# Kernel optimization log

Hardware: AMD Instinct MI355X
Metric: run time of the kernel (lower is better)

Reference implementation:

```python
import jax, jax.numpy as jnp
import numpy as np

D_MODEL = 256
B, BS_ANT, UE_ANT, N_SC = 4, 64, 4, 512
LN_EPS = 1e-5


def _xavier(key, shape, gain):
    fan_out, fan_in = shape
    bound = gain * np.sqrt(6.0 / (fan_in + fan_out))
    return jax.random.uniform(key, shape, jnp.float32, -bound, bound)


def setup_inputs() -> dict:
    key = jax.random.key(0)
    ks = jax.random.split(key, 8)
    csi_real = jax.random.normal(ks[0], (B, BS_ANT, UE_ANT, N_SC), jnp.float32)
    csi_imag = jax.random.normal(ks[1], (B, BS_ANT, UE_ANT, N_SC), jnp.float32)
    return {
        "csi_real": csi_real,
        "csi_imag": csi_imag,
        "w_c": _xavier(ks[2], (D_MODEL, 2), 2.0),
        "b_c": jnp.zeros((D_MODEL,), jnp.float32),
        "w_s": _xavier(ks[3], (D_MODEL, 1), 1.0),
        "b_s": jnp.zeros((D_MODEL,), jnp.float32),
        "w_u": _xavier(ks[4], (D_MODEL, 1), 1.0),
        "b_u": jnp.zeros((D_MODEL,), jnp.float32),
        "w_f": _xavier(ks[5], (D_MODEL, 1), 1.0),
        "b_f": jnp.zeros((D_MODEL,), jnp.float32),
        "ln_gamma": jnp.ones((D_MODEL,), jnp.float32),
        "ln_beta": jnp.zeros((D_MODEL,), jnp.float32),
    }


def reference(csi_real, csi_imag, w_c, b_c, w_s, b_s, w_u, b_u, w_f, b_f, ln_gamma, ln_beta):
    bs_ant, ue_ant, n_sc = csi_real.shape[1], csi_real.shape[2], csi_real.shape[3]
    # complex projection: stack(real, imag) @ W_c^T + b_c, done without the stack
    x = csi_real[..., None] * w_c[:, 0] + csi_imag[..., None] * w_c[:, 1] + b_c  # [B,BS,UE,SC,D]
    # index embeddings computed on the small per-axis arange, then broadcast (same math
    # as projecting the fully-expanded index tensors, since the projection is affine)
    sp = jnp.arange(bs_ant, dtype=csi_real.dtype)[:, None] * w_s[:, 0] + b_s   # [BS,D]
    ue = jnp.arange(ue_ant, dtype=csi_real.dtype)[:, None] * w_u[:, 0] + b_u   # [UE,D]
    fr = jnp.arange(n_sc, dtype=csi_real.dtype)[:, None] * w_f[:, 0] + b_f     # [SC,D]
    x = x + sp[None, :, None, None, :] + ue[None, None, :, None, :] + fr[None, None, None, :, :]
    # LayerNorm over d_model
    mu = jnp.mean(x, axis=-1, keepdims=True)
    xc = x - mu
    var = jnp.mean(xc * xc, axis=-1, keepdims=True)
    x = xc * jax.lax.rsqrt(var + LN_EPS) * ln_gamma + ln_beta
    # dropout is identity in eval/reference mode
    return x
```

## Files before the change

kernel.cpp:

```cpp
#include <hip/hip_runtime.h>

#define D_MODEL 256
#define LN_EPS 1e-5f
#define NWAVES 8192
#define NITER  64

typedef float f4 __attribute__((ext_vector_type(4)));

__device__ __forceinline__ float rfl(float x) {
    return __uint_as_float(__builtin_amdgcn_readfirstlane(__float_as_uint(x)));
}

__global__ __launch_bounds__(256, 8) void csi_encoder_kernel(
    const float* __restrict__ csi_real,
    const float* __restrict__ csi_imag,
    const float* __restrict__ w_c,
    const float* __restrict__ b_c,
    const float* __restrict__ w_s,
    const float* __restrict__ b_s,
    const float* __restrict__ w_u,
    const float* __restrict__ b_u,
    const float* __restrict__ w_f,
    const float* __restrict__ b_f,
    const float* __restrict__ ln_gamma,
    const float* __restrict__ ln_beta,
    float* __restrict__ out)
{
    const int lane = threadIdx.x & 63;
    const int waveId = blockIdx.x * 4 + (threadIdx.x >> 6);
    const int w0 = __builtin_amdgcn_readfirstlane(waveId);

    const float fS = (float)(w0 & 511);
    const float fU = (float)((w0 >> 9) & 3);
    const int   b0 = (w0 >> 11) & 63;

    const int d0 = lane * 4;
    float a0[4], a1[4], aB[4], w2[4], gv[4], bv[4];
#pragma unroll
    for (int j = 0; j < 4; ++j) {
        const int d = d0 + j;
        a0[j] = w_c[d * 2 + 0];
        a1[j] = w_c[d * 2 + 1];
        aB[j] = w_s[d];
        const float bsum = b_c[d] + b_s[d] + b_u[d] + b_f[d];
        w2[j] = fmaf(fS, w_f[d], fmaf(fU, w_u[d], bsum));
        gv[j] = ln_gamma[d];
        bv[j] = ln_beta[d];
    }

    float p[14];
#pragma unroll
    for (int i = 0; i < 14; ++i) p[i] = 0.0f;
#pragma unroll
    for (int j = 0; j < 4; ++j) {
        p[0]  = fmaf(a0[j], a0[j], p[0]);
        p[1]  = fmaf(a1[j], a1[j], p[1]);
        p[2]  = fmaf(aB[j], aB[j], p[2]);
        p[3]  = fmaf(w2[j], w2[j], p[3]);
        p[4]  = fmaf(a0[j], a1[j], p[4]);
        p[5]  = fmaf(a0[j], aB[j], p[5]);
        p[6]  = fmaf(a0[j], w2[j], p[6]);
        p[7]  = fmaf(a1[j], aB[j], p[7]);
        p[8]  = fmaf(a1[j], w2[j], p[8]);
        p[9]  = fmaf(aB[j], w2[j], p[9]);
        p[10] += a0[j];
        p[11] += a1[j];
        p[12] += aB[j];
        p[13] += w2[j];
    }
#pragma unroll
    for (int off = 32; off >= 1; off >>= 1) {
#pragma unroll
        for (int i = 0; i < 14; ++i) p[i] += __shfl_xor(p[i], off, 64);
    }

    const float inv = 1.0f / 256.0f;
    const float E00 = rfl(p[0] * inv);
    const float E11 = rfl(p[1] * inv);
    const float EBB = rfl(p[2] * inv);
    const float E33 = rfl(p[3] * inv);
    const float F01 = rfl(2.0f * p[4] * inv);
    const float F0B = rfl(2.0f * p[5] * inv);
    const float F03 = rfl(2.0f * p[6] * inv);
    const float F1B = rfl(2.0f * p[7] * inv);
    const float F13 = rfl(2.0f * p[8] * inv);
    const float FB3 = rfl(2.0f * p[9] * inv);
    const float M0  = rfl(p[10] * inv);
    const float M1  = rfl(p[11] * inv);
    const float MB  = rfl(p[12] * inv);
    const float M3  = rfl(p[13] * inv);

    const float* __restrict__ cr = csi_real + w0;
    const float* __restrict__ ci = csi_imag + w0;
    float* __restrict__ op = out + (size_t)w0 * D_MODEL + d0;

#pragma unroll 4
    for (int i = 0; i < NITER; ++i) {
        const float re = cr[(size_t)i << 13];
        const float im = ci[(size_t)i << 13];
        const float fB = (float)((b0 + 4 * i) & 63);

        const float mu = fmaf(M0, re, fmaf(M1, im, fmaf(MB, fB, M3)));
        const float ms = fmaf(re, fmaf(E00, re, fmaf(F01, im, fmaf(F0B, fB, F03))),
                         fmaf(im, fmaf(E11, im, fmaf(F1B, fB, F13)),
                         fmaf(fB, fmaf(EBB, fB, FB3), E33)));
        const float var  = fmaf(-mu, mu, ms);
        const float rstd = rsqrtf(var + LN_EPS);

        f4 o;
#pragma unroll
        for (int k = 0; k < 4; ++k) {
            const float t = fmaf(re, a0[k], fmaf(im, a1[k], fmaf(fB, aB[k], w2[k])));
            o[k] = fmaf((t - mu) * rstd, gv[k], bv[k]);
        }
        __builtin_nontemporal_store(o, (f4*)(op + ((size_t)i << 13) * D_MODEL));
    }
}

extern "C" void kernel_launch(void* const* d_in, const int* in_sizes, int n_in,
                              void* d_out, int out_size, void* d_ws, size_t ws_size,
                              hipStream_t stream) {
    const float* csi_real = (const float*)d_in[0];
    const float* csi_imag = (const float*)d_in[1];
    const float* w_c      = (const float*)d_in[2];
    const float* b_c      = (const float*)d_in[3];
    const float* w_s      = (const float*)d_in[4];
    const float* b_s      = (const float*)d_in[5];
    const float* w_u      = (const float*)d_in[6];
    const float* b_u      = (const float*)d_in[7];
    const float* w_f      = (const float*)d_in[8];
    const float* b_f      = (const float*)d_in[9];
    const float* ln_gamma = (const float*)d_in[10];
    const float* ln_beta  = (const float*)d_in[11];
    float* out = (float*)d_out;

    csi_encoder_kernel<<<2048, 256, 0, stream>>>(
        csi_real, csi_imag, w_c, b_c, w_s, b_s, w_u, b_u, w_f, b_f,
        ln_gamma, ln_beta, out);
}
```

Baseline: 120.8 us.

## Assign fewer waves more rows each, folding UE index into per-row stats

Measured after the change: 158.3 us. 31.1% more time.

```diff
diff --git a/kernel.cpp b/kernel.cpp
--- a/kernel.cpp
+++ b/kernel.cpp
@@ -2,8 +2,8 @@
 
 #define D_MODEL 256
 #define LN_EPS 1e-5f
-#define NWAVES 8192
-#define NITER  64
+#define NWAVES 1024
+#define NITER  512
 
 typedef float f4 __attribute__((ext_vector_type(4)));
 
@@ -11,7 +11,7 @@
     return __uint_as_float(__builtin_amdgcn_readfirstlane(__float_as_uint(x)));
 }
 
-__global__ __launch_bounds__(256, 8) void csi_encoder_kernel(
+__global__ __launch_bounds__(256) void csi_encoder_kernel(
     const float* __restrict__ csi_real,
     const float* __restrict__ csi_imag,
     const float* __restrict__ w_c,
@@ -27,94 +27,134 @@
     float* __restrict__ out)
 {
     const int lane = threadIdx.x & 63;
-    const int waveId = blockIdx.x * 4 + (threadIdx.x >> 6);
-    const int w0 = __builtin_amdgcn_readfirstlane(waveId);
+    const int w0 = __builtin_amdgcn_readfirstlane(blockIdx.x * 4 + (threadIdx.x >> 6));
 
-    const float fS = (float)(w0 & 511);
-    const float fU = (float)((w0 >> 9) & 3);
-    const int   b0 = (w0 >> 11) & 63;
+    const float fS  = (float)(w0 & 511);
+    const int  bit9 = (w0 >> 9) & 1;
+    const float fU0 = (float)bit9;
+    const float fU1 = (float)(bit9 + 2);
 
     const int d0 = lane * 4;
-    float a0[4], a1[4], aB[4], w2[4], gv[4], bv[4];
+    float a0[4], a1[4], aU[4], aB[4], w2[4], gv[4], bv[4];
 #pragma unroll
     for (int j = 0; j < 4; ++j) {
         const int d = d0 + j;
         a0[j] = w_c[d * 2 + 0];
         a1[j] = w_c[d * 2 + 1];
+        aU[j] = w_u[d];
         aB[j] = w_s[d];
         const float bsum = b_c[d] + b_s[d] + b_u[d] + b_f[d];
-        w2[j] = fmaf(fS, w_f[d], fmaf(fU, w_u[d], bsum));
+        w2[j] = fmaf(fS, w_f[d], bsum);
         gv[j] = ln_gamma[d];
         bv[j] = ln_beta[d];
     }
 
-    float p[14];
+    float p[20];
 #pragma unroll
-    for (int i = 0; i < 14; ++i) p[i] = 0.0f;
+    for (int i = 0; i < 20; ++i) p[i] = 0.0f;
 #pragma unroll
     for (int j = 0; j < 4; ++j) {
         p[0]  = fmaf(a0[j], a0[j], p[0]);
         p[1]  = fmaf(a1[j], a1[j], p[1]);
-        p[2]  = fmaf(aB[j], aB[j], p[2]);
-        p[3]  = fmaf(w2[j], w2[j], p[3]);
-        p[4]  = fmaf(a0[j], a1[j], p[4]);
-        p[5]  = fmaf(a0[j], aB[j], p[5]);
-        p[6]  = fmaf(a0[j], w2[j], p[6]);
-        p[7]  = fmaf(a1[j], aB[j], p[7]);
-        p[8]  = fmaf(a1[j], w2[j], p[8]);
-        p[9]  = fmaf(aB[j], w2[j], p[9]);
-        p[10] += a0[j];
-        p[11] += a1[j];
-        p[12] += aB[j];
-        p[13] += w2[j];
+        p[2]  = fmaf(aU[j], aU[j], p[2]);
+        p[3]  = fmaf(aB[j], aB[j], p[3]);
+        p[4]  = fmaf(w2[j], w2[j], p[4]);
+        p[5]  = fmaf(a0[j], a1[j], p[5]);
+        p[6]  = fmaf(a0[j], aU[j], p[6]);
+        p[7]  = fmaf(a0[j], aB[j], p[7]);
+        p[8]  = fmaf(a0[j], w2[j], p[8]);
+        p[9]  = fmaf(a1[j], aU[j], p[9]);
+        p[10] = fmaf(a1[j], aB[j], p[10]);
+        p[11] = fmaf(a1[j], w2[j], p[11]);
+        p[12] = fmaf(aU[j], aB[j], p[12]);
+        p[13] = fmaf(aU[j], w2[j], p[13]);
+        p[14] = fmaf(aB[j], w2[j], p[14]);
+        p[15] += a0[j];
+        p[16] += a1[j];
+        p[17] += aU[j];
+        p[18] += aB[j];
+        p[19] += w2[j];
     }
 #pragma unroll
     for (int off = 32; off >= 1; off >>= 1) {
 #pragma unroll
-        for (int i = 0; i < 14; ++i) p[i] += __shfl_xor(p[i], off, 64);
+        for (int i = 0; i < 20; ++i) p[i] += __shfl_xor(p[i], off, 64);
     }
 
     const float inv = 1.0f / 256.0f;
     const float E00 = rfl(p[0] * inv);
     const float E11 = rfl(p[1] * inv);
-    const float EBB = rfl(p[2] * inv);
-    const float E33 = rfl(p[3] * inv);
-    const float F01 = rfl(2.0f * p[4] * inv);
-    const float F0B = rfl(2.0f * p[5] * inv);
-    const float F03 = rfl(2.0f * p[6] * inv);
-    const float F1B = rfl(2.0f * p[7] * inv);
-    const float F13 = rfl(2.0f * p[8] * inv);
-    const float FB3 = rfl(2.0f * p[9] * inv);
-    const float M0  = rfl(p[10] * inv);
-    const float M1  = rfl(p[11] * inv);
-    const float MB  = rfl(p[12] * inv);
-    const float M3  = rfl(p[13] * inv);
+    const float EUU = rfl(p[2] * inv);
+    const float EBB = rfl(p[3] * inv);
+    const float Eww = rfl(p[4] * inv);
+    const float F01 = rfl(2.0f * p[5]  * inv);
+    const float F0U = rfl(2.0f * p[6]  * inv);
+    const float F0B = rfl(2.0f * p[7]  * inv);
+    const float F0w = rfl(2.0f * p[8]  * inv);
+    const float F1U = rfl(2.0f * p[9]  * inv);
+    const float F1B = rfl(2.0f * p[10] * inv);
+    const float F1w = rfl(2.0f * p[11] * inv);
+    const float FUB = rfl(2.0f * p[12] * inv);
+    const float FUw = rfl(2.0f * p[13] * inv);
+    const float FBw = rfl(2.0f * p[14] * inv);
+    const float M0  = rfl(p[15] * inv);
+    const float M1  = rfl(p[16] * inv);
+    const float MU  = rfl(p[17] * inv);
+    const float MB  = rfl(p[18] * inv);
+    const float Mw  = rfl(p[19] * inv);
 
     const float* __restrict__ cr = csi_real + w0;
     const float* __restrict__ ci = csi_imag + w0;
     float* __restrict__ op = out + (size_t)w0 * D_MODEL + d0;
 
-#pragma unroll 4
-    for (int i = 0; i < NITER; ++i) {
-        const float re = cr[(size_t)i << 13];
-        const float im = ci[(size_t)i << 13];
-        const float fB = (float)((b0 + 4 * i) & 63);
-
-        const float mu = fmaf(M0, re, fmaf(M1, im, fmaf(MB, fB, M3)));
-        const float ms = fmaf(re, fmaf(E00, re, fmaf(F01, im, fmaf(F0B, fB, F03))),
-                         fmaf(im, fmaf(E11, im, fmaf(F1B, fB, F13)),
-                         fmaf(fB, fmaf(EBB, fB, FB3), E33)));
-        const float var  = fmaf(-mu, mu, ms);
-        const float rstd = rsqrtf(var + LN_EPS);
-
-        f4 o;
+    auto process = [&](int b, const float* re4, const float* im4) {
+        const float fBa = (float)((2 * b) & 63);
+        const float fBb = (float)((2 * b + 1) & 63);
 #pragma unroll
         for (int k = 0; k < 4; ++k) {
-            const float t = fmaf(re, a0[k], fmaf(im, a1[k], fmaf(fB, aB[k], w2[k])));
-            o[k] = fmaf((t - mu) * rstd, gv[k], bv[k]);
+            const float re = re4[k];
+            const float im = im4[k];
+            const float fU = (k & 1) ? fU1 : fU0;
+            const float fB = (k >> 1) ? fBb : fBa;
+
+            const float mu = fmaf(M0, re, fmaf(M1, im,
+                             fmaf(MU, fU, fmaf(MB, fB, Mw))));
+            const float ms = fmaf(re, fmaf(E00, re, fmaf(F01, im, fmaf(F0U, fU, fmaf(F0B, fB, F0w)))),
+                             fmaf(im, fmaf(E11, im, fmaf(F1U, fU, fmaf(F1B, fB, F1w))),
+                             fmaf(fU, fmaf(EUU, fU, fmaf(FUB, fB, FUw)),
+                             fmaf(fB, fmaf(EBB, fB, FBw), Eww))));
+            const float var  = fmaf(-mu, mu, ms);
+            const float rstd = rsqrtf(var + LN_EPS);
+
+            f4 o;
+#pragma unroll
+            for (int kk = 0; kk < 4; ++kk) {
+                const float t = fmaf(re, a0[kk], fmaf(im, a1[kk],
+                                fmaf(fU, aU[kk], fmaf(fB, aB[kk], w2[kk]))));
+                o[kk] = fmaf((t - mu) * rstd, gv[kk], bv[kk]);
+            }
+            *reinterpret_cast<f4*>(op + ((size_t)(4 * b + k) << 18)) = o;
         }
-        __builtin_nontemporal_store(o, (f4*)(op + ((size_t)i << 13) * D_MODEL));
+    };
+
+    float cre[4], cim[4];
+#pragma unroll
+    for (int k = 0; k < 4; ++k) {
+        cre[k] = cr[(size_t)k << 10];
+        cim[k] = ci[(size_t)k << 10];
     }
+    for (int b = 0; b < 127; ++b) {
+        float nre[4], nim[4];
+#pragma unroll
+        for (int k = 0; k < 4; ++k) {
+            nre[k] = cr[(size_t)(4 * b + 4 + k) << 10];
+            nim[k] = ci[(size_t)(4 * b + 4 + k) << 10];
+        }
+        process(b, cre, cim);
+#pragma unroll
+        for (int k = 0; k < 4; ++k) { cre[k] = nre[k]; cim[k] = nim[k]; }
+    }
+    process(127, cre, cim);
 }
 
 extern "C" void kernel_launch(void* const* d_in, const int* in_sizes, int n_in,
@@ -134,7 +174,7 @@
     const float* ln_beta  = (const float*)d_in[11];
     float* out = (float*)d_out;
 
-    csi_encoder_kernel<<<2048, 256, 0, stream>>>(
+    csi_encoder_kernel<<<256, 256, 0, stream>>>(
         csi_real, csi_imag, w_c, b_c, w_s, b_s, w_u, b_u, w_f, b_f,
         ln_gamma, ln_beta, out);
 }
```
